# Kernel tuning notes

Hardware: AMD Instinct MI355X
Metric: run time of the kernel (lower is better)

Reference implementation:

```python
import jax, jax.numpy as jnp
import numpy as np

DIM = 512
NUM_GROUPS = 32
NUM_HEADS = 8
EPS = 1e-5


def group_norm(x, gamma, beta):
    # x: (B, C, H, W); normalize over (C//G, H, W) per group
    B, C, H, W = x.shape
    g = x.reshape(B, NUM_GROUPS, -1)
    mean = g.mean(axis=2, keepdims=True)
    var = g.var(axis=2, keepdims=True)
    g = (g - mean) * jax.lax.rsqrt(var + EPS)
    x = g.reshape(B, C, H, W)
    return x * gamma[None, :, None, None] + beta[None, :, None, None]


def setup_inputs() -> dict:
    key = jax.random.key(0)
    ks = jax.random.split(key, 7)
    B, C, H, W = 16, DIM, 32, 32
    x = jax.random.normal(ks[0], (B, C, H, W), dtype=jnp.float32)
    gamma = jnp.ones((C,), dtype=jnp.float32)
    beta = jnp.zeros((C,), dtype=jnp.float32)
    s_in = 1.0 / np.sqrt(C)
    w_qkv = jax.random.normal(ks[1], (3 * C, C), dtype=jnp.float32) * s_in
    b_qkv = jnp.zeros((3 * C,), dtype=jnp.float32)
    w_proj = jax.random.normal(ks[2], (C, C), dtype=jnp.float32) * s_in
    b_proj = jnp.zeros((C,), dtype=jnp.float32)
    return {"x": x, "gamma": gamma, "beta": beta, "w_qkv": w_qkv,
            "b_qkv": b_qkv, "w_proj": w_proj, "b_proj": b_proj}


def reference(x, gamma, beta, w_qkv, b_qkv, w_proj, b_proj):
    B, C, H, W = x.shape
    nh = NUM_HEADS
    c3 = 3 * C // nh          # per-head qkv channels (3 * head_dim)
    dh = C // nh              # head_dim
    scale = C ** (-0.5)       # NOTE: source scales by full dim, not head_dim

    h = group_norm(x, gamma, beta)

    # 1x1 conv qkv projection: (B, 3C, H, W)
    qkv = jnp.einsum('bchw,oc->bohw', h, w_qkv) + b_qkv[None, :, None, None]

    # rearrange 'b (head c) h w -> (b head) (h w) c'
    qkv = qkv.reshape(B, nh, c3, H, W)
    qkv = qkv.transpose(0, 1, 3, 4, 2).reshape(B * nh, H * W, c3)
    q, k, v = jnp.split(qkv, 3, axis=2)   # each (B*nh, HW, dh)

    score = jnp.einsum('bnc,bmc->bnm', q, k * scale)   # (B*nh, HW, HW)
    attn = jax.nn.softmax(score, axis=2)
    out = jnp.einsum('bnm,bmc->bnc', attn, v)          # (B*nh, HW, dh)

    # rearrange '(head b) (h w) c -> b (head c) h w'  (NOTE head-major, as in source)
    out = out.reshape(nh, B, H, W, dh)
    out = out.transpose(1, 0, 4, 2, 3).reshape(B, C, H, W)

    out = jnp.einsum('bchw,oc->bohw', out, w_proj) + b_proj[None, :, None, None]
    return out + x
```

## Files before the change

### kernel.cpp

```cpp
#include <hip/hip_runtime.h>
#include <stdint.h>

typedef __bf16 bf16;
typedef __attribute__((ext_vector_type(4))) float f32x4;
typedef __attribute__((ext_vector_type(8))) __bf16 bf16x8;
typedef __attribute__((ext_vector_type(4))) __bf16 bf16x4;

#define NB 16
#define CH 512
#define HWS 1024
#define NHEAD 8
#define DH 64
#define O3 1536
#define LDP 72
#define CPQ 136
#define CPF 132

__device__ __forceinline__ void gload_lds16(const bf16* g, bf16* l) {
    __builtin_amdgcn_global_load_lds(
        (const __attribute__((address_space(1))) unsigned int*)g,
        (__attribute__((address_space(3))) unsigned int*)l,
        16, 0, 0);
}

#if defined(__has_builtin) && __has_builtin(__builtin_amdgcn_exp2f)
__device__ __forceinline__ float fast_exp2(float x) { return __builtin_amdgcn_exp2f(x); }
#else
__device__ __forceinline__ float fast_exp2(float x) { return exp2f(x); }
#endif

__global__ void prep(const float* __restrict__ x, float* __restrict__ stats,
                     const float* __restrict__ wq, const float* __restrict__ wp,
                     bf16* __restrict__ wq_b, bf16* __restrict__ wp_b) {
    int bx = blockIdx.x;
    if (bx < 512) {
        int b = bx >> 5, g = bx & 31;
        const float4* p = (const float4*)(x + ((size_t)(b * CH + g * 16)) * HWS);
        float s = 0.f, ss = 0.f;
        for (int i = threadIdx.x; i < 4096; i += 256) {
            float4 v = p[i];
            s  += v.x + v.y + v.z + v.w;
            ss += v.x*v.x + v.y*v.y + v.z*v.z + v.w*v.w;
        }
        for (int off = 32; off; off >>= 1) {
            s  += __shfl_xor(s,  off, 64);
            ss += __shfl_xor(ss, off, 64);
        }
        __shared__ float red[8];
        int w = threadIdx.x >> 6;
        if ((threadIdx.x & 63) == 0) { red[w*2] = s; red[w*2+1] = ss; }
        __syncthreads();
        if (threadIdx.x == 0) {
            float S  = red[0] + red[2] + red[4] + red[6];
            float SS = red[1] + red[3] + red[5] + red[7];
            float mean = S * (1.f/16384.f);
            float var  = SS * (1.f/16384.f) - mean*mean;
            stats[bx*2]   = mean;
            stats[bx*2+1] = rsqrtf(var + 1e-5f);
        }
    } else {
        int i = (bx - 512) * 256 + threadIdx.x;
        if (i < O3*CH) wq_b[i] = (bf16)wq[i];
        else           wp_b[i - O3*CH] = (bf16)wp[i - O3*CH];
    }
}

__global__ void gn_apply_t(const float* __restrict__ x, const float* __restrict__ stats,
                           const float* __restrict__ gamma, const float* __restrict__ beta,
                           bf16* __restrict__ hT) {
    __shared__ float tile[32][33];
    int bx = blockIdx.x;
    int b = bx >> 9;
    int rem = bx & 511;
    int ct = rem >> 5, nt = rem & 31;
    int tx = threadIdx.x & 31, ty = threadIdx.x >> 5;
    #pragma unroll
    for (int r = 0; r < 4; ++r) {
        int c = ct*32 + ty + r*8;
        int n = nt*32 + tx;
        float v = x[((size_t)(b * CH + c)) * HWS + n];
        int g = c >> 4;
        float mean = stats[(b*32+g)*2], rstd = stats[(b*32+g)*2+1];
        tile[ty + r*8][tx] = (v - mean) * rstd * gamma[c] + beta[c];
    }
    __syncthreads();
    #pragma unroll
    for (int r = 0; r < 4; ++r) {
        int n = nt*32 + ty + r*8;
        int c = ct*32 + tx;
        hT[((size_t)(b * HWS + n)) * CH + c] = (bf16)tile[tx][ty + r*8];
    }
}

__global__ __launch_bounds__(256, 3)
void qkv_gemm(const bf16* __restrict__ W, const bf16* __restrict__ hT,
              const float* __restrict__ bias, bf16* __restrict__ qkv,
              bf16* __restrict__ vT) {
    __shared__ __align__(16) bf16 SMEM[128*CPQ];
    bf16* As = SMEM;
    bf16* Bs = SMEM + 8192;
    int bx = blockIdx.x;
    int po = bx >> 7, qo = bx & 127;
    int obase = po*128, bnbase = qo*128;
    int tid = threadIdx.x;
    int lane = tid & 63, w = tid >> 6;
    int quad = lane >> 4, l15 = lane & 15;
    int wm = w >> 1, wn = w & 1;
    int x7 = l15 & 7;
    int srow = lane >> 3, spos = lane & 7;
    int sgc = (spos ^ srow) * 8;

    f32x4 acc[4][4] = {};
    for (int k0 = 0; k0 < 512; k0 += 64) {
        #pragma unroll
        for (int r = 0; r < 4; ++r) {
            int rb = r*32 + w*8;
            gload_lds16(W  + ((size_t)(obase  + rb + srow))*512 + k0 + sgc, &As[rb*64]);
            gload_lds16(hT + ((size_t)(bnbase + rb + srow))*512 + k0 + sgc, &Bs[rb*64]);
        }
        __syncthreads();
        #pragma unroll
        for (int ks = 0; ks < 2; ++ks) {
            int ch = (ks*4 + quad) ^ x7;
            bf16x8 af[4], bfv[4];
            #pragma unroll
            for (int mt = 0; mt < 4; ++mt)
                af[mt] = *(const bf16x8*)(&As[(wm*64 + mt*16 + l15)*64 + ch*8]);
            #pragma unroll
            for (int nt = 0; nt < 4; ++nt)
                bfv[nt] = *(const bf16x8*)(&Bs[(wn*64 + nt*16 + l15)*64 + ch*8]);
            #pragma unroll
            for (int mt = 0; mt < 4; ++mt)
                #pragma unroll
                for (int nt = 0; nt < 4; ++nt)
                    acc[mt][nt] = __builtin_amdgcn_mfma_f32_16x16x32_bf16(af[mt], bfv[nt], acc[mt][nt], 0, 0, 0);
        }
        __syncthreads();
    }

    bf16* Cs = SMEM;
    int b = bnbase >> 10;
    int nbase = bnbase & 1023;
    #pragma unroll
    for (int mt = 0; mt < 4; ++mt) {
        int o0 = obase + wm*64 + mt*16 + quad*4;
        float4 bb = *(const float4*)(bias + o0);
        int c192 = o0 % 192;
        bool isV = (c192 >= 128);
        int h = o0 / 192;
        int d0 = c192 - 128;
        #pragma unroll
        for (int nt = 0; nt < 4; ++nt) {
            int bn_l = wn*64 + nt*16 + l15;
            bf16x4 v;
            v[0] = (bf16)(acc[mt][nt][0] + bb.x);
            v[1] = (bf16)(acc[mt][nt][1] + bb.y);
            v[2] = (bf16)(acc[mt][nt][2] + bb.z);
            v[3] = (bf16)(acc[mt][nt][3] + bb.w);
            *(bf16x4*)(&Cs[bn_l*CPQ + (o0 - obase)]) = v;
            if (isV) {
                int key = nbase + bn_l;
                size_t vb_ = ((size_t)((b*8 + h)*64 + d0)) * HWS + key;
                vT[vb_]          = v[0];
                vT[vb_ + HWS]    = v[1];
                vT[vb_ + 2*HWS]  = v[2];
                vT[vb_ + 3*HWS]  = v[3];
            }
        }
    }
    __syncthreads();
    #pragma unroll
    for (int p = 0; p < 8; ++p) {
        int bn_l = p*16 + (tid >> 4);
        int o8 = (tid & 15) * 8;
        if ((obase + o8) % 192 < 128) {
            uint4 v = *(const uint4*)(&Cs[bn_l*CPQ + o8]);
            *(uint4*)(qkv + ((size_t)(bnbase + bn_l)) * O3 + obase + o8) = v;
        }
    }
}

__global__ __launch_bounds__(256, 4)
void flash_attn(const bf16* __restrict__ qkv, const bf16* __restrict__ vT,
                bf16* __restrict__ A2) {
    __shared__ __align__(16) bf16 Ks[64*LDP];
    __shared__ __align__(16) bf16 Vs[64*LDP];
    __shared__ __align__(16) bf16 Ps[4][32*LDP];
    int bx = blockIdx.x;
    int g = bx & 127, qt = bx >> 7;
    int b = g >> 3, h = g & 7;
    int tid = threadIdx.x, lane = tid & 63, w = tid >> 6;
    int quad = lane >> 4, l15 = lane & 15;
    const float kLog2 = 0.04419417382415922f * 1.44269504088896341f;

    bf16x8 aq[2][2];
    #pragma unroll
    for (int mt = 0; mt < 2; ++mt) {
        int qrow = qt*128 + w*32 + mt*16 + l15;
        const bf16* qb = qkv + ((size_t)(b * HWS + qrow)) * O3 + h*192;
        aq[mt][0] = *(const bf16x8*)(qb + quad*8);
        aq[mt][1] = *(const bf16x8*)(qb + 32 + quad*8);
        #pragma unroll
        for (int j = 0; j < 8; ++j) {
            aq[mt][0][j] = (bf16)((float)aq[mt][0][j] * kLog2);
            aq[mt][1][j] = (bf16)((float)aq[mt][1][j] * kLog2);
        }
    }

    f32x4 acc[2][4] = {};
    f32x4 L4[2] = {};

    int r0 = tid >> 3, d0 = (tid & 7) * 8;
    int r1 = r0 + 32;
    const bf16* kp0 = qkv + ((size_t)(b * HWS + r0)) * O3 + h*192 + 64 + d0;
    const bf16* kp1 = qkv + ((size_t)(b * HWS + r1)) * O3 + h*192 + 64 + d0;
    const bf16* vp0 = vT + ((size_t)(g * DH + r0)) * HWS + d0;
    const bf16* vp1 = vT + ((size_t)(g * DH + r1)) * HWS + d0;
    bf16* ksd0 = &Ks[r0*LDP + d0];
    bf16* ksd1 = &Ks[r1*LDP + d0];
    bf16* vsd0 = &Vs[r0*LDP + d0];
    bf16* vsd1 = &Vs[r1*LDP + d0];

    uint4 ka = *(const uint4*)(kp0);
    uint4 kb = *(const uint4*)(kp1);
    uint4 va = *(const uint4*)(vp0);
    uint4 vb = *(const uint4*)(vp1);

    for (int kt = 0; kt < 16; ++kt) {
        __syncthreads();
        *(uint4*)ksd0 = ka;
        *(uint4*)ksd1 = kb;
        *(uint4*)vsd0 = va;
        *(uint4*)vsd1 = vb;
        __syncthreads();
        if (kt < 15) {
            size_t ko = (size_t)(kt+1) * 64 * O3;
            size_t vo = (size_t)(kt+1) * 64;
            ka = *(const uint4*)(kp0 + ko);
            kb = *(const uint4*)(kp1 + ko);
            va = *(const uint4*)(vp0 + vo);
            vb = *(const uint4*)(vp1 + vo);
        }

        #pragma unroll
        for (int nt = 0; nt < 4; ++nt) {
            bf16x8 ak0 = *(const bf16x8*)(&Ks[(nt*16 + l15)*LDP + quad*8]);
            bf16x8 ak1 = *(const bf16x8*)(&Ks[(nt*16 + l15)*LDP + 32 + quad*8]);
            #pragma unroll
            for (int mt = 0; mt < 2; ++mt) {
                f32x4 z = {};
                z = __builtin_amdgcn_mfma_f32_16x16x32_bf16(ak0, aq[mt][0], z, 0, 0, 0);
                z = __builtin_amdgcn_mfma_f32_16x16x32_bf16(ak1, aq[mt][1], z, 0, 0, 0);
                bf16x4 p;
                #pragma unroll
                for (int r = 0; r < 4; ++r) {
                    float e = fast_exp2(z[r]);
                    L4[mt][r] += e;
                    p[r] = (bf16)e;
                }
                *(bf16x4*)(&Ps[w][(mt*16 + l15)*LDP + nt*16 + quad*4]) = p;
            }
        }
        bf16x8 ap[2][2];
        #pragma unroll
        for (int mt = 0; mt < 2; ++mt) {
            ap[mt][0] = *(const bf16x8*)(&Ps[w][(mt*16 + l15)*LDP + quad*8]);
            ap[mt][1] = *(const bf16x8*)(&Ps[w][(mt*16 + l15)*LDP + 32 + quad*8]);
        }
        #pragma unroll
        for (int dt = 0; dt < 4; ++dt) {
            bf16x8 bv0 = *(const bf16x8*)(&Vs[(dt*16 + l15)*LDP + quad*8]);
            bf16x8 bv1 = *(const bf16x8*)(&Vs[(dt*16 + l15)*LDP + 32 + quad*8]);
            #pragma unroll
            for (int mt = 0; mt < 2; ++mt) {
                acc[mt][dt] = __builtin_amdgcn_mfma_f32_16x16x32_bf16(ap[mt][0], bv0, acc[mt][dt], 0, 0, 0);
                acc[mt][dt] = __builtin_amdgcn_mfma_f32_16x16x32_bf16(ap[mt][1], bv1, acc[mt][dt], 0, 0, 0);
            }
        }
    }

    float Linv[2][4];
    #pragma unroll
    for (int mt = 0; mt < 2; ++mt) {
        float Lf = (L4[mt][0] + L4[mt][1]) + (L4[mt][2] + L4[mt][3]);
        Lf += __shfl_xor(Lf, 16, 64);
        Lf += __shfl_xor(Lf, 32, 64);
        #pragma unroll
        for (int r = 0; r < 4; ++r)
            Linv[mt][r] = 1.f / __shfl(Lf, quad*4 + r, 64);
    }

    __syncthreads();
    #pragma unroll
    for (int mt = 0; mt < 2; ++mt)
        #pragma unroll
        for (int dt = 0; dt < 4; ++dt)
            #pragma unroll
            for (int r = 0; r < 4; ++r)
                Ps[w][(mt*16 + quad*4 + r)*LDP + dt*16 + l15] = (bf16)(acc[mt][dt][r] * Linv[mt][r]);

    int bp = g & 15;
    int hp = g >> 4;
    #pragma unroll
    for (int cc = 0; cc < 4; ++cc) {
        int c = cc*64 + lane;
        int row = c >> 3, dcc = c & 7;
        uint4 v = *(const uint4*)(&Ps[w][row*LDP + dcc*8]);
        size_t idx = ((size_t)(bp * HWS + qt*128 + w*32 + row)) * CH + hp*64 + dcc*8;
        *(uint4*)(A2 + idx) = v;
    }
}

__global__ __launch_bounds__(256, 3)
void proj_gemm(const bf16* __restrict__ A2, const bf16* __restrict__ Wp,
               const float* __restrict__ bias, const float* __restrict__ x,
               float* __restrict__ out) {
    __shared__ __align__(16) bf16 SMEM[16896];
    bf16* As = SMEM;
    bf16* Bs = SMEM + 8192;
    int bx = blockIdx.x;
    int po = bx >> 7, qo = bx & 127;
    int obase = po*128, bnbase = qo*128;
    int tid = threadIdx.x;
    int lane = tid & 63, w = tid >> 6;
    int quad = lane >> 4, l15 = lane & 15;
    int wm = w >> 1, wn = w & 1;
    int x7 = l15 & 7;
    int srow = lane >> 3, spos = lane & 7;
    int sgc = (spos ^ srow) * 8;

    f32x4 acc[4][4] = {};
    for (int k0 = 0; k0 < 512; k0 += 64) {
        #pragma unroll
        for (int r = 0; r < 4; ++r) {
            int rb = r*32 + w*8;
            gload_lds16(A2 + ((size_t)(bnbase + rb + srow))*512 + k0 + sgc, &As[rb*64]);
            gload_lds16(Wp + ((size_t)(obase  + rb + srow))*512 + k0 + sgc, &Bs[rb*64]);
        }
        __syncthreads();
        #pragma unroll
        for (int ks = 0; ks < 2; ++ks) {
            int ch = (ks*4 + quad) ^ x7;
            bf16x8 af[4], bfv[4];
            #pragma unroll
            for (int mt = 0; mt < 4; ++mt)
                af[mt] = *(const bf16x8*)(&As[(wm*64 + mt*16 + l15)*64 + ch*8]);
            #pragma unroll
            for (int nt = 0; nt < 4; ++nt)
                bfv[nt] = *(const bf16x8*)(&Bs[(wn*64 + nt*16 + l15)*64 + ch*8]);
            #pragma unroll
            for (int mt = 0; mt < 4; ++mt)
                #pragma unroll
                for (int nt = 0; nt < 4; ++nt)
                    acc[mt][nt] = __builtin_amdgcn_mfma_f32_16x16x32_bf16(af[mt], bfv[nt], acc[mt][nt], 0, 0, 0);
        }
        __syncthreads();
    }

    float* Cf = (float*)SMEM;
    int bb = bnbase >> 10;
    int nbase = bnbase & 1023;
    #pragma unroll
    for (int hh = 0; hh < 2; ++hh) {
        if (wm == hh) {
            #pragma unroll
            for (int mt = 0; mt < 4; ++mt)
                #pragma unroll
                for (int nt = 0; nt < 4; ++nt)
                    #pragma unroll
                    for (int r = 0; r < 4; ++r)
                        Cf[(mt*16 + quad*4 + r)*CPF + wn*64 + nt*16 + l15] = acc[mt][nt][r];
        }
        __syncthreads();
        #pragma unroll
        for (int p = 0; p < 4; ++p) {
            int ol = p*32 + (tid >> 3);
            int nl0 = (tid & 7) * 8;
            int o = obase + ol;
            float bv = bias[o];
            #pragma unroll
            for (int jj = 0; jj < 2; ++jj) {
                int nl = nl0 + jj*4;
                size_t idx = ((size_t)(bb * CH + o)) * HWS + nbase + hh*64 + nl;
                float4 xr = *(const float4*)(x + idx);
                float4 res;
                res.x = Cf[(nl+0)*CPF + ol] + bv + xr.x;
                res.y = Cf[(nl+1)*CPF + ol] + bv + xr.y;
                res.z = Cf[(nl+2)*CPF + ol] + bv + xr.z;
                res.w = Cf[(nl+3)*CPF + ol] + bv + xr.w;
                *(float4*)(out + idx) = res;
            }
        }
        __syncthreads();
    }
}

extern "C" void kernel_launch(void* const* d_in, const int* in_sizes, int n_in,
                              void* d_out, int out_size, void* d_ws, size_t ws_size,
                              hipStream_t stream) {
    const float* x      = (const float*)d_in[0];
    const float* gamma  = (const float*)d_in[1];
    const float* beta   = (const float*)d_in[2];
    const float* w_qkv  = (const float*)d_in[3];
    const float* b_qkv  = (const float*)d_in[4];
    const float* w_proj = (const float*)d_in[5];
    const float* b_proj = (const float*)d_in[6];
    float* out = (float*)d_out;

    char* ws = (char*)d_ws;
    float* stats = (float*)(ws + 0);
    bf16*  wq_b  = (bf16*)(ws + 4096);
    bf16*  wp_b  = (bf16*)(ws + 1576960);
    bf16*  hT    = (bf16*)(ws + 2101248);
    bf16*  qkv   = (bf16*)(ws + 18878464);
    bf16*  vT    = (bf16*)(ws + 69210112);
    bf16*  A2    = hT;

    prep       <<<4608, 256, 0, stream>>>(x, stats, w_qkv, w_proj, wq_b, wp_b);
    gn_apply_t <<<8192, 256, 0, stream>>>(x, stats, gamma, beta, hT);
    qkv_gemm   <<<1536, 256, 0, stream>>>(wq_b, hT, b_qkv, qkv, vT);
    flash_attn <<<1024, 256, 0, stream>>>(qkv, vT, A2);
    proj_gemm  <<<512,  256, 0, stream>>>(A2, wp_b, b_proj, x, out);
}
```

Baseline: 204.8 us.

## Load K/V MFMA fragments directly from global memory instead of LDS staging

The flash attention kernel no longer stages K and V tiles through shared memory with block-wide barriers. Each wave now loads its MFMA operand fragments for K and V straight from global memory, relying on L1/L2 caching across the four waves. This removes the LDS traffic and both __syncthreads per iteration, and adds s_setprio around MFMA groups. In exchange each K/V element is read from global or cache four times (once per wave), and the register-prefetch double buffering is gone, so load latency is more exposed.

```diff
diff --git a/kernel.cpp b/kernel.cpp
--- a/kernel.cpp
+++ b/kernel.cpp
@@ -183,8 +183,6 @@
 __global__ __launch_bounds__(256, 4)
 void flash_attn(const bf16* __restrict__ qkv, const bf16* __restrict__ vT,
                 bf16* __restrict__ A2) {
-    __shared__ __align__(16) bf16 Ks[64*LDP];
-    __shared__ __align__(16) bf16 Vs[64*LDP];
     __shared__ __align__(16) bf16 Ps[4][32*LDP];
     int bx = blockIdx.x;
     int g = bx & 127, qt = bx >> 7;
@@ -210,47 +208,23 @@
     f32x4 acc[2][4] = {};
     f32x4 L4[2] = {};
 
-    int r0 = tid >> 3, d0 = (tid & 7) * 8;
-    int r1 = r0 + 32;
-    const bf16* kp0 = qkv + ((size_t)(b * HWS + r0)) * O3 + h*192 + 64 + d0;
-    const bf16* kp1 = qkv + ((size_t)(b * HWS + r1)) * O3 + h*192 + 64 + d0;
-    const bf16* vp0 = vT + ((size_t)(g * DH + r0)) * HWS + d0;
-    const bf16* vp1 = vT + ((size_t)(g * DH + r1)) * HWS + d0;
-    bf16* ksd0 = &Ks[r0*LDP + d0];
-    bf16* ksd1 = &Ks[r1*LDP + d0];
-    bf16* vsd0 = &Vs[r0*LDP + d0];
-    bf16* vsd1 = &Vs[r1*LDP + d0];
-
-    uint4 ka = *(const uint4*)(kp0);
-    uint4 kb = *(const uint4*)(kp1);
-    uint4 va = *(const uint4*)(vp0);
-    uint4 vb = *(const uint4*)(vp1);
+    const bf16* kb0 = qkv + ((size_t)(b * HWS + l15)) * O3 + h*192 + 64 + quad*8;
+    const bf16* vb0 = vT + ((size_t)(g * DH + l15)) * HWS + quad*8;
 
     for (int kt = 0; kt < 16; ++kt) {
-        __syncthreads();
-        *(uint4*)ksd0 = ka;
-        *(uint4*)ksd1 = kb;
-        *(uint4*)vsd0 = va;
-        *(uint4*)vsd1 = vb;
-        __syncthreads();
-        if (kt < 15) {
-            size_t ko = (size_t)(kt+1) * 64 * O3;
-            size_t vo = (size_t)(kt+1) * 64;
-            ka = *(const uint4*)(kp0 + ko);
-            kb = *(const uint4*)(kp1 + ko);
-            va = *(const uint4*)(vp0 + vo);
-            vb = *(const uint4*)(vp1 + vo);
-        }
-
+        const bf16* kkt = kb0 + (size_t)(kt*64) * O3;
         #pragma unroll
         for (int nt = 0; nt < 4; ++nt) {
-            bf16x8 ak0 = *(const bf16x8*)(&Ks[(nt*16 + l15)*LDP + quad*8]);
-            bf16x8 ak1 = *(const bf16x8*)(&Ks[(nt*16 + l15)*LDP + 32 + quad*8]);
+            const bf16* kp = kkt + (size_t)(nt*16) * O3;
+            bf16x8 ak0 = *(const bf16x8*)(kp);
+            bf16x8 ak1 = *(const bf16x8*)(kp + 32);
             #pragma unroll
             for (int mt = 0; mt < 2; ++mt) {
                 f32x4 z = {};
+                __builtin_amdgcn_s_setprio(1);
                 z = __builtin_amdgcn_mfma_f32_16x16x32_bf16(ak0, aq[mt][0], z, 0, 0, 0);
                 z = __builtin_amdgcn_mfma_f32_16x16x32_bf16(ak1, aq[mt][1], z, 0, 0, 0);
+                __builtin_amdgcn_s_setprio(0);
                 bf16x4 p;
                 #pragma unroll
                 for (int r = 0; r < 4; ++r) {
@@ -269,13 +243,16 @@
         }
         #pragma unroll
         for (int dt = 0; dt < 4; ++dt) {
-            bf16x8 bv0 = *(const bf16x8*)(&Vs[(dt*16 + l15)*LDP + quad*8]);
-            bf16x8 bv1 = *(const bf16x8*)(&Vs[(dt*16 + l15)*LDP + 32 + quad*8]);
+            const bf16* vp = vb0 + (size_t)(dt*16) * HWS + kt*64;
+            bf16x8 bv0 = *(const bf16x8*)(vp);
+            bf16x8 bv1 = *(const bf16x8*)(vp + 32);
+            __builtin_amdgcn_s_setprio(1);
             #pragma unroll
             for (int mt = 0; mt < 2; ++mt) {
                 acc[mt][dt] = __builtin_amdgcn_mfma_f32_16x16x32_bf16(ap[mt][0], bv0, acc[mt][dt], 0, 0, 0);
                 acc[mt][dt] = __builtin_amdgcn_mfma_f32_16x16x32_bf16(ap[mt][1], bv1, acc[mt][dt], 0, 0, 0);
             }
+            __builtin_amdgcn_s_setprio(0);
         }
     }
 
@@ -290,7 +267,6 @@
             Linv[mt][r] = 1.f / __shfl(Lf, quad*4 + r, 64);
     }
 
-    __syncthreads();
     #pragma unroll
     for (int mt = 0; mt < 2; ++mt)
         #pragma unroll
```

After: 274.8 us. 34.2% more time.
